# Performance work log

Measured on AMD Instinct MI355X. Metric: run time of the kernel, lower is better.

## Reference

```python
import jax, jax.numpy as jnp
import numpy as np

B, C, H, W = 1024, 1024, 14, 14
A = 8          # adt_num (number of expert branches)
CH = C // 4    # expert bottleneck width


def setup_inputs() -> dict:
    key = jax.random.key(0)
    ks = jax.random.split(key, 5)
    s_in = 1.0 / np.sqrt(C)
    s_hid = 1.0 / np.sqrt(CH)
    return {
        "features": jax.random.normal(ks[0], (B, C, H, W), dtype=jnp.float32),
        "fc_w": jax.random.normal(ks[1], (A, C), dtype=jnp.float32) * s_in,
        "fc_b": jnp.zeros((A,), dtype=jnp.float32),
        "fc1_w": jax.random.normal(ks[2], (A, C, CH), dtype=jnp.float32) * s_in,
        "fc1_b": jnp.zeros((A, CH), dtype=jnp.float32),
        "fc2_w": jax.random.normal(ks[3], (A, CH, C), dtype=jnp.float32) * s_hid,
        "fc2_b": jnp.zeros((A, C), dtype=jnp.float32),
    }


def reference(features, fc_w, fc_b, fc1_w, fc1_b, fc2_w, fc2_b):
    # Global average pool over spatial dims: [B, C]
    pooled = jnp.mean(features.reshape(features.shape[0], features.shape[1], -1), axis=2)
    # All adt_num expert branches as one batched GEMM pair: [B, A, CH] -> [B, A, C]
    h = jax.nn.relu(jnp.einsum("bc,ach->bah", pooled, fc1_w) + fc1_b)
    expert = jnp.einsum("bah,ahc->bac", h, fc2_w) + fc2_b
    # Softmax gating over experts: [B, A]
    gate = jax.nn.softmax(pooled @ fc_w.T + fc_b, axis=1)
    # Gate-weighted sum of expert outputs: [B, C]
    mixed = jnp.einsum("ba,bac->bc", gate, expert)
    # Sigmoid channel gate + residual: out = x * sigmoid(mixed) + x
    scale = jax.nn.sigmoid(mixed)[:, :, None, None]
    return features * scale + features
```

## Files before the change

kernel.cpp:

```cpp
#include <hip/hip_runtime.h>

#define B_  1024
#define C_  1024
#define HW_ 196
#define A_  8
#define CH_ 256
#define N1_ 2048
#define K2_ 2048

typedef __attribute__((ext_vector_type(8))) short short8;
typedef __attribute__((ext_vector_type(4))) float f32x4;

static __device__ __forceinline__ unsigned short f2bf(float x) {
  union { float f; unsigned u; } v; v.f = x;
  unsigned r = (v.u + 0x7FFFu + ((v.u >> 16) & 1u)) >> 16;
  return (unsigned short)r;
}

__global__ __launch_bounds__(256) void pool_k(const float* __restrict__ f,
                                              float* __restrict__ pooled,
                                              unsigned short* __restrict__ pooledb) {
  int wid = (blockIdx.x * 256 + threadIdx.x) >> 6;
  int lane = threadIdx.x & 63;
  unsigned row0 = (unsigned)wid * 64;
  const f32x4* base = (const f32x4*)f;
  #pragma unroll 2
  for (int it = 0; it < 64; ++it) {
    unsigned row = row0 + it;
    float s = 0.f;
    if (lane < 49) {
      f32x4 v = __builtin_nontemporal_load(&base[(size_t)row * 49 + lane]);
      s = v.x + v.y + v.z + v.w;
    }
    #pragma unroll
    for (int off = 32; off > 0; off >>= 1) s += __shfl_down(s, off, 64);
    if (lane == 0) {
      float m = s * (1.0f / 196.0f);
      pooled[row] = m;
      pooledb[row] = f2bf(m);
    }
  }
}

__global__ void gate_k(const float* __restrict__ pooled, const float* __restrict__ fc_w,
                       const float* __restrict__ fc_b, float* __restrict__ gate) {
  __shared__ float dots[A_];
  int b = blockIdx.x;
  int wave = threadIdx.x >> 6, lane = threadIdx.x & 63;
  const float* p = pooled + (size_t)b * C_;
  for (int e = wave; e < A_; e += 4) {
    const float* wrow = fc_w + (size_t)e * C_;
    float sum = 0.f;
    for (int c = lane; c < C_; c += 64) sum += p[c] * wrow[c];
    #pragma unroll
    for (int off = 32; off > 0; off >>= 1) sum += __shfl_down(sum, off, 64);
    if (lane == 0) dots[e] = sum + fc_b[e];
  }
  __syncthreads();
  if (threadIdx.x == 0) {
    float mx = dots[0];
    for (int e = 1; e < A_; ++e) mx = fmaxf(mx, dots[e]);
    float ex[A_], se = 0.f;
    for (int e = 0; e < A_; ++e) { ex[e] = __expf(dots[e] - mx); se += ex[e]; }
    float inv = 1.0f / se;
    for (int e = 0; e < A_; ++e) gate[(size_t)b * A_ + e] = ex[e] * inv;
  }
}

__global__ void tconv_k(const float* __restrict__ fc1_w, const float* __restrict__ fc2_w,
                        unsigned short* __restrict__ w1t, unsigned short* __restrict__ w2t) {
  __shared__ float tile[32][33];
  int t = blockIdx.x;
  const float* in; unsigned short* out; int Cc, OS, c0, r0;
  if (t < 2048) {
    int z = t >> 8, rem = t & 255;
    in  = fc1_w + (size_t)z * (C_ * CH_);
    out = w1t   + (size_t)z * (CH_ * C_);
    Cc = CH_; OS = C_;
    c0 = (rem & 7) * 32;  r0 = (rem >> 3) * 32;
  } else {
    t -= 2048;
    int z = t >> 8, rem = t & 255;
    in  = fc2_w + (size_t)z * (CH_ * C_);
    out = w2t   + (size_t)z * CH_;
    Cc = C_; OS = K2_;
    c0 = (rem & 31) * 32; r0 = (rem >> 5) * 32;
  }
  int tx = threadIdx.x & 31, ty = threadIdx.x >> 5;
  #pragma unroll
  for (int i = 0; i < 32; i += 8)
    tile[ty + i][tx] = in[(size_t)(r0 + ty + i) * Cc + c0 + tx];
  __syncthreads();
  #pragma unroll
  for (int i = 0; i < 32; i += 8)
    out[(size_t)(c0 + ty + i) * OS + r0 + tx] = f2bf(tile[tx][ty + i]);
}

__global__ __launch_bounds__(256) void gemm1_k(const unsigned short* __restrict__ Ab,
                                               const unsigned short* __restrict__ Bt,
                                               const float* __restrict__ fc1_b,
                                               const float* __restrict__ gate,
                                               unsigned short* __restrict__ gh) {
  int w = threadIdx.x >> 6, lane = threadIdx.x & 63;
  int r = lane & 15, kg = lane >> 4;
  int brow = blockIdx.x * 64 + (w >> 1) * 32;
  int bcol = blockIdx.y * 64 + (w & 1) * 32;
  const short8* Ap0 = (const short8*)(Ab + (size_t)(brow + r) * C_ + kg * 8);
  const short8* Ap1 = (const short8*)(Ab + (size_t)(brow + 16 + r) * C_ + kg * 8);
  const short8* Bp0 = (const short8*)(Bt + (size_t)(bcol + r) * C_ + kg * 8);
  const short8* Bp1 = (const short8*)(Bt + (size_t)(bcol + 16 + r) * C_ + kg * 8);
  f32x4 acc[2][2];
  acc[0][0] = (f32x4){0,0,0,0}; acc[0][1] = acc[0][0];
  acc[1][0] = acc[0][0];        acc[1][1] = acc[0][0];
  #pragma unroll 4
  for (int k = 0; k < C_ / 32; ++k) {
    short8 a0 = Ap0[4 * k], a1 = Ap1[4 * k];
    short8 b0 = Bp0[4 * k], b1 = Bp1[4 * k];
    acc[0][0] = __builtin_amdgcn_mfma_f32_16x16x32_bf16(a0, b0, acc[0][0], 0, 0, 0);
    acc[0][1] = __builtin_amdgcn_mfma_f32_16x16x32_bf16(a0, b1, acc[0][1], 0, 0, 0);
    acc[1][0] = __builtin_amdgcn_mfma_f32_16x16x32_bf16(a1, b0, acc[1][0], 0, 0, 0);
    acc[1][1] = __builtin_amdgcn_mfma_f32_16x16x32_bf16(a1, b1, acc[1][1], 0, 0, 0);
  }
  #pragma unroll
  for (int mi = 0; mi < 2; ++mi)
    #pragma unroll
    for (int ni = 0; ni < 2; ++ni) {
      int col = bcol + ni * 16 + r;
      int aidx = col >> 8;
      float bias = fc1_b[col];
      #pragma unroll
      for (int reg = 0; reg < 4; ++reg) {
        int row = brow + mi * 16 + kg * 4 + reg;
        float val = acc[mi][ni][reg] + bias;
        val = fmaxf(val, 0.f) * gate[row * A_ + aidx];
        gh[(size_t)row * N1_ + col] = f2bf(val);
      }
    }
}

__global__ __launch_bounds__(256) void gemm2_k(const unsigned short* __restrict__ Ab,
                                               const unsigned short* __restrict__ Bt,
                                               const float* __restrict__ gate,
                                               const float* __restrict__ fc2_b,
                                               float* __restrict__ s_out) {
  int w = threadIdx.x >> 6, lane = threadIdx.x & 63;
  int r = lane & 15, kg = lane >> 4;
  int brow = blockIdx.x * 64 + (w >> 1) * 32;
  int bcol = blockIdx.y * 64 + (w & 1) * 32;
  const short8* Ap0 = (const short8*)(Ab + (size_t)(brow + r) * K2_ + kg * 8);
  const short8* Ap1 = (const short8*)(Ab + (size_t)(brow + 16 + r) * K2_ + kg * 8);
  const short8* Bp0 = (const short8*)(Bt + (size_t)(bcol + r) * K2_ + kg * 8);
  const short8* Bp1 = (const short8*)(Bt + (size_t)(bcol + 16 + r) * K2_ + kg * 8);
  f32x4 acc[2][2];
  acc[0][0] = (f32x4){0,0,0,0}; acc[0][1] = acc[0][0];
  acc[1][0] = acc[0][0];        acc[1][1] = acc[0][0];
  #pragma unroll 4
  for (int k = 0; k < K2_ / 32; ++k) {
    short8 a0 = Ap0[4 * k], a1 = Ap1[4 * k];
    short8 b0 = Bp0[4 * k], b1 = Bp1[4 * k];
    acc[0][0] = __builtin_amdgcn_mfma_f32_16x16x32_bf16(a0, b0, acc[0][0], 0, 0, 0);
    acc[0][1] = __builtin_amdgcn_mfma_f32_16x16x32_bf16(a0, b1, acc[0][1], 0, 0, 0);
    acc[1][0] = __builtin_amdgcn_mfma_f32_16x16x32_bf16(a1, b0, acc[1][0], 0, 0, 0);
    acc[1][1] = __builtin_amdgcn_mfma_f32_16x16x32_bf16(a1, b1, acc[1][1], 0, 0, 0);
  }
  #pragma unroll
  for (int mi = 0; mi < 2; ++mi)
    #pragma unroll
    for (int ni = 0; ni < 2; ++ni) {
      int col = bcol + ni * 16 + r;
      float b8[A_];
      #pragma unroll
      for (int a = 0; a < A_; ++a) b8[a] = fc2_b[a * C_ + col];
      #pragma unroll
      for (int reg = 0; reg < 4; ++reg) {
        int row = brow + mi * 16 + kg * 4 + reg;
        const float* g = gate + (size_t)row * A_;
        float bias = 0.f;
        #pragma unroll
        for (int a = 0; a < A_; ++a) bias += g[a] * b8[a];
        float mixed = acc[mi][ni][reg] + bias;
        s_out[(size_t)row * C_ + col] = 1.0f + 1.0f / (1.0f + __expf(-mixed));
      }
    }
}

__global__ __launch_bounds__(256) void apply_k(const f32x4* __restrict__ f,
                                               const float* __restrict__ s,
                                               f32x4* __restrict__ out, unsigned total4) {
  unsigned i = blockIdx.x * 256 + threadIdx.x;
  unsigned stride = gridDim.x * 256;
  for (; i < total4; i += stride) {
    f32x4 v = __builtin_nontemporal_load(&f[i]);
    float m = s[i / 49u];
    v *= m;
    __builtin_nontemporal_store(v, &out[i]);
  }
}

extern "C" void kernel_launch(void* const* d_in, const int* in_sizes, int n_in,
                              void* d_out, int out_size, void* d_ws, size_t ws_size,
                              hipStream_t stream) {
  const float* features = (const float*)d_in[0];
  const float* fc_w  = (const float*)d_in[1];
  const float* fc_b  = (const float*)d_in[2];
  const float* fc1_w = (const float*)d_in[3];
  const float* fc1_b = (const float*)d_in[4];
  const float* fc2_w = (const float*)d_in[5];
  const float* fc2_b = (const float*)d_in[6];
  float* out = (float*)d_out;
  char* ws = (char*)d_ws;

  float*          pooled  = (float*)(ws);
  unsigned short* pooledb = (unsigned short*)(ws + 0x400000);
  float*          gate    = (float*)(ws + 0x600000);
  unsigned short* gh      = (unsigned short*)(ws + 0x610000);
  unsigned short* w1t     = (unsigned short*)(ws + 0xA10000);
  unsigned short* w2t     = (unsigned short*)(ws + 0xE10000);
  float*          s_buf   = (float*)(ws + 0x1210000);

  pool_k<<<4096, 256, 0, stream>>>(features, pooled, pooledb);
  gate_k<<<B_, 256, 0, stream>>>(pooled, fc_w, fc_b, gate);
  tconv_k<<<4096, 256, 0, stream>>>(fc1_w, fc2_w, w1t, w2t);
  gemm1_k<<<dim3(16, 32), 256, 0, stream>>>(pooledb, w1t, fc1_b, gate, gh);
  gemm2_k<<<dim3(16, 16), 256, 0, stream>>>(gh, w2t, gate, fc2_b, s_buf);
  apply_k<<<8192, 256, 0, stream>>>((const f32x4*)features, s_buf, (f32x4*)out,
                                    (unsigned)(out_size / 4));
}
```

Measured before the change: 555.6 us.

## Merge pooling and weight transpose-convert into one launch with batched row reduction

```diff
diff --git a/kernel.cpp b/kernel.cpp
--- a/kernel.cpp
+++ b/kernel.cpp
@@ -10,6 +10,7 @@
 
 typedef __attribute__((ext_vector_type(8))) short short8;
 typedef __attribute__((ext_vector_type(4))) float f32x4;
+typedef __attribute__((ext_vector_type(4))) unsigned short us4;
 
 static __device__ __forceinline__ unsigned short f2bf(float x) {
   union { float f; unsigned u; } v; v.f = x;
@@ -17,28 +18,71 @@
   return (unsigned short)r;
 }
 
-__global__ __launch_bounds__(256) void pool_k(const float* __restrict__ f,
-                                              float* __restrict__ pooled,
-                                              unsigned short* __restrict__ pooledb) {
-  int wid = (blockIdx.x * 256 + threadIdx.x) >> 6;
-  int lane = threadIdx.x & 63;
-  unsigned row0 = (unsigned)wid * 64;
-  const f32x4* base = (const f32x4*)f;
-  #pragma unroll 2
-  for (int it = 0; it < 64; ++it) {
-    unsigned row = row0 + it;
-    float s = 0.f;
-    if (lane < 49) {
-      f32x4 v = __builtin_nontemporal_load(&base[(size_t)row * 49 + lane]);
-      s = v.x + v.y + v.z + v.w;
-    }
-    #pragma unroll
-    for (int off = 32; off > 0; off >>= 1) s += __shfl_down(s, off, 64);
-    if (lane == 0) {
-      float m = s * (1.0f / 196.0f);
-      pooled[row] = m;
-      pooledb[row] = f2bf(m);
-    }
+__global__ __launch_bounds__(256) void pooltc_k(const float* __restrict__ f,
+                                                float* __restrict__ pooled,
+                                                unsigned short* __restrict__ pooledb,
+                                                const float* __restrict__ fc1_w,
+                                                const float* __restrict__ fc2_w,
+                                                unsigned short* __restrict__ w1t,
+                                                unsigned short* __restrict__ w2t) {
+  __shared__ float tile[32][33];
+  if (blockIdx.x < 4096) {
+    int wid = (blockIdx.x * 256 + threadIdx.x) >> 6;
+    int lane = threadIdx.x & 63;
+    int lc = lane < 49 ? lane : 48;
+    float msk = lane < 49 ? 1.0f : 0.0f;
+    unsigned row0 = (unsigned)wid * 64;
+    const f32x4* base = (const f32x4*)f;
+    for (int it = 0; it < 64; it += 4) {
+      unsigned row = row0 + it;
+      f32x4 v0 = base[(size_t)(row + 0) * 49 + lc];
+      f32x4 v1 = base[(size_t)(row + 1) * 49 + lc];
+      f32x4 v2 = base[(size_t)(row + 2) * 49 + lc];
+      f32x4 v3 = base[(size_t)(row + 3) * 49 + lc];
+      float s0 = (v0.x + v0.y + v0.z + v0.w) * msk;
+      float s1 = (v1.x + v1.y + v1.z + v1.w) * msk;
+      float s2 = (v2.x + v2.y + v2.z + v2.w) * msk;
+      float s3 = (v3.x + v3.y + v3.z + v3.w) * msk;
+      #pragma unroll
+      for (int off = 32; off > 0; off >>= 1) {
+        s0 += __shfl_xor(s0, off, 64);
+        s1 += __shfl_xor(s1, off, 64);
+        s2 += __shfl_xor(s2, off, 64);
+        s3 += __shfl_xor(s3, off, 64);
+      }
+      if (lane == 0) {
+        f32x4 m = {s0, s1, s2, s3};
+        m *= (1.0f / 196.0f);
+        *(f32x4*)&pooled[row] = m;
+        us4 mb = {f2bf(m.x), f2bf(m.y), f2bf(m.z), f2bf(m.w)};
+        *(us4*)&pooledb[row] = mb;
+      }
+    }
+  } else {
+    int t = blockIdx.x - 4096;
+    const float* in; unsigned short* out; int Cc, OS, c0, r0;
+    if (t < 2048) {
+      int z = t >> 8, rem = t & 255;
+      in  = fc1_w + (size_t)z * (C_ * CH_);
+      out = w1t   + (size_t)z * (CH_ * C_);
+      Cc = CH_; OS = C_;
+      c0 = (rem & 7) * 32;  r0 = (rem >> 3) * 32;
+    } else {
+      t -= 2048;
+      int z = t >> 8, rem = t & 255;
+      in  = fc2_w + (size_t)z * (CH_ * C_);
+      out = w2t   + (size_t)z * CH_;
+      Cc = C_; OS = K2_;
+      c0 = (rem & 31) * 32; r0 = (rem >> 5) * 32;
+    }
+    int tx = threadIdx.x & 31, ty = threadIdx.x >> 5;
+    #pragma unroll
+    for (int i = 0; i < 32; i += 8)
+      tile[ty + i][tx] = in[(size_t)(r0 + ty + i) * Cc + c0 + tx];
+    __syncthreads();
+    #pragma unroll
+    for (int i = 0; i < 32; i += 8)
+      out[(size_t)(c0 + ty + i) * OS + r0 + tx] = f2bf(tile[tx][ty + i]);
   }
 }
 
@@ -65,35 +109,6 @@
     float inv = 1.0f / se;
     for (int e = 0; e < A_; ++e) gate[(size_t)b * A_ + e] = ex[e] * inv;
   }
-}
-
-__global__ void tconv_k(const float* __restrict__ fc1_w, const float* __restrict__ fc2_w,
-                        unsigned short* __restrict__ w1t, unsigned short* __restrict__ w2t) {
-  __shared__ float tile[32][33];
-  int t = blockIdx.x;
-  const float* in; unsigned short* out; int Cc, OS, c0, r0;
-  if (t < 2048) {
-    int z = t >> 8, rem = t & 255;
-    in  = fc1_w + (size_t)z * (C_ * CH_);
-    out = w1t   + (size_t)z * (CH_ * C_);
-    Cc = CH_; OS = C_;
-    c0 = (rem & 7) * 32;  r0 = (rem >> 3) * 32;
-  } else {
-    t -= 2048;
-    int z = t >> 8, rem = t & 255;
-    in  = fc2_w + (size_t)z * (CH_ * C_);
-    out = w2t   + (size_t)z * CH_;
-    Cc = C_; OS = K2_;
-    c0 = (rem & 31) * 32; r0 = (rem >> 5) * 32;
-  }
-  int tx = threadIdx.x & 31, ty = threadIdx.x >> 5;
-  #pragma unroll
-  for (int i = 0; i < 32; i += 8)
-    tile[ty + i][tx] = in[(size_t)(r0 + ty + i) * Cc + c0 + tx];
-  __syncthreads();
-  #pragma unroll
-  for (int i = 0; i < 32; i += 8)
-    out[(size_t)(c0 + ty + i) * OS + r0 + tx] = f2bf(tile[tx][ty + i]);
 }
 
 __global__ __launch_bounds__(256) void gemm1_k(const unsigned short* __restrict__ Ab,
@@ -218,9 +233,8 @@
   unsigned short* w2t     = (unsigned short*)(ws + 0xE10000);
   float*          s_buf   = (float*)(ws + 0x1210000);
 
-  pool_k<<<4096, 256, 0, stream>>>(features, pooled, pooledb);
+  pooltc_k<<<8192, 256, 0, stream>>>(features, pooled, pooledb, fc1_w, fc2_w, w1t, w2t);
   gate_k<<<B_, 256, 0, stream>>>(pooled, fc_w, fc_b, gate);
-  tconv_k<<<4096, 256, 0, stream>>>(fc1_w, fc2_w, w1t, w2t);
   gemm1_k<<<dim3(16, 32), 256, 0, stream>>>(pooledb, w1t, fc1_b, gate, gh);
   gemm2_k<<<dim3(16, 16), 256, 0, stream>>>(gh, w2t, gate, fc2_b, s_buf);
   apply_k<<<8192, 256, 0, stream>>>((const f32x4*)features, s_buf, (f32x4*)out,
```

Result: no change. 553.2 us (-0.4%).

## Fuse pooling and weight transpose-convert into one launch, thread-per-row pooling

Applied to the files above, without the earlier changes.

```diff
diff --git a/kernel.cpp b/kernel.cpp
--- a/kernel.cpp
+++ b/kernel.cpp
@@ -17,28 +17,56 @@
   return (unsigned short)r;
 }
 
-__global__ __launch_bounds__(256) void pool_k(const float* __restrict__ f,
-                                              float* __restrict__ pooled,
-                                              unsigned short* __restrict__ pooledb) {
-  int wid = (blockIdx.x * 256 + threadIdx.x) >> 6;
-  int lane = threadIdx.x & 63;
-  unsigned row0 = (unsigned)wid * 64;
-  const f32x4* base = (const f32x4*)f;
-  #pragma unroll 2
-  for (int it = 0; it < 64; ++it) {
-    unsigned row = row0 + it;
+__global__ __launch_bounds__(256) void pooltc_k(const float* __restrict__ f,
+                                                float* __restrict__ pooled,
+                                                unsigned short* __restrict__ pooledb,
+                                                const float* __restrict__ fc1_w,
+                                                const float* __restrict__ fc2_w,
+                                                unsigned short* __restrict__ w1t,
+                                                unsigned short* __restrict__ w2t) {
+  __shared__ float tile[32][33];
+  if (blockIdx.x < 4096) {
+    unsigned row = blockIdx.x * 256 + threadIdx.x;
+    const f32x4* p = (const f32x4*)f + (size_t)row * 49;
     float s = 0.f;
-    if (lane < 49) {
-      f32x4 v = __builtin_nontemporal_load(&base[(size_t)row * 49 + lane]);
-      s = v.x + v.y + v.z + v.w;
-    }
-    #pragma unroll
-    for (int off = 32; off > 0; off >>= 1) s += __shfl_down(s, off, 64);
-    if (lane == 0) {
-      float m = s * (1.0f / 196.0f);
-      pooled[row] = m;
-      pooledb[row] = f2bf(m);
-    }
+    #pragma unroll 3
+    for (int j = 0; j < 12; ++j) {
+      f32x4 a = p[4 * j + 0], b = p[4 * j + 1], c = p[4 * j + 2], d = p[4 * j + 3];
+      s += (a.x + a.y) + (a.z + a.w);
+      s += (b.x + b.y) + (b.z + b.w);
+      s += (c.x + c.y) + (c.z + c.w);
+      s += (d.x + d.y) + (d.z + d.w);
+    }
+    f32x4 e = p[48];
+    s += (e.x + e.y) + (e.z + e.w);
+    float m = s * (1.0f / 196.0f);
+    pooled[row] = m;
+    pooledb[row] = f2bf(m);
+  } else {
+    int t = blockIdx.x - 4096;
+    const float* in; unsigned short* out; int Cc, OS, c0, r0;
+    if (t < 2048) {
+      int z = t >> 8, rem = t & 255;
+      in  = fc1_w + (size_t)z * (C_ * CH_);
+      out = w1t   + (size_t)z * (CH_ * C_);
+      Cc = CH_; OS = C_;
+      c0 = (rem & 7) * 32;  r0 = (rem >> 3) * 32;
+    } else {
+      t -= 2048;
+      int z = t >> 8, rem = t & 255;
+      in  = fc2_w + (size_t)z * (CH_ * C_);
+      out = w2t   + (size_t)z * CH_;
+      Cc = C_; OS = K2_;
+      c0 = (rem & 31) * 32; r0 = (rem >> 5) * 32;
+    }
+    int tx = threadIdx.x & 31, ty = threadIdx.x >> 5;
+    #pragma unroll
+    for (int i = 0; i < 32; i += 8)
+      tile[ty + i][tx] = in[(size_t)(r0 + ty + i) * Cc + c0 + tx];
+    __syncthreads();
+    #pragma unroll
+    for (int i = 0; i < 32; i += 8)
+      out[(size_t)(c0 + ty + i) * OS + r0 + tx] = f2bf(tile[tx][ty + i]);
   }
 }
 
@@ -65,35 +93,6 @@
     float inv = 1.0f / se;
     for (int e = 0; e < A_; ++e) gate[(size_t)b * A_ + e] = ex[e] * inv;
   }
-}
-
-__global__ void tconv_k(const float* __restrict__ fc1_w, const float* __restrict__ fc2_w,
-                        unsigned short* __restrict__ w1t, unsigned short* __restrict__ w2t) {
-  __shared__ float tile[32][33];
-  int t = blockIdx.x;
-  const float* in; unsigned short* out; int Cc, OS, c0, r0;
-  if (t < 2048) {
-    int z = t >> 8, rem = t & 255;
-    in  = fc1_w + (size_t)z * (C_ * CH_);
-    out = w1t   + (size_t)z * (CH_ * C_);
-    Cc = CH_; OS = C_;
-    c0 = (rem & 7) * 32;  r0 = (rem >> 3) * 32;
-  } else {
-    t -= 2048;
-    int z = t >> 8, rem = t & 255;
-    in  = fc2_w + (size_t)z * (CH_ * C_);
-    out = w2t   + (size_t)z * CH_;
-    Cc = C_; OS = K2_;
-    c0 = (rem & 31) * 32; r0 = (rem >> 5) * 32;
-  }
-  int tx = threadIdx.x & 31, ty = threadIdx.x >> 5;
-  #pragma unroll
-  for (int i = 0; i < 32; i += 8)
-    tile[ty + i][tx] = in[(size_t)(r0 + ty + i) * Cc + c0 + tx];
-  __syncthreads();
-  #pragma unroll
-  for (int i = 0; i < 32; i += 8)
-    out[(size_t)(c0 + ty + i) * OS + r0 + tx] = f2bf(tile[tx][ty + i]);
 }
 
 __global__ __launch_bounds__(256) void gemm1_k(const unsigned short* __restrict__ Ab,
@@ -218,9 +217,8 @@
   unsigned short* w2t     = (unsigned short*)(ws + 0xE10000);
   float*          s_buf   = (float*)(ws + 0x1210000);
 
-  pool_k<<<4096, 256, 0, stream>>>(features, pooled, pooledb);
+  pooltc_k<<<8192, 256, 0, stream>>>(features, pooled, pooledb, fc1_w, fc2_w, w1t, w2t);
   gate_k<<<B_, 256, 0, stream>>>(pooled, fc_w, fc_b, gate);
-  tconv_k<<<4096, 256, 0, stream>>>(fc1_w, fc2_w, w1t, w2t);
   gemm1_k<<<dim3(16, 32), 256, 0, stream>>>(pooledb, w1t, fc1_b, gate, gh);
   gemm2_k<<<dim3(16, 16), 256, 0, stream>>>(gh, w2t, gate, fc2_b, s_buf);
   apply_k<<<8192, 256, 0, stream>>>((const f32x4*)features, s_buf, (f32x4*)out,
```

Measured after the change: 554.5 us. About the same (-0.2%).
